# Kernel optimization log

Measured on AMD Instinct MI355X. Metric: run time of the kernel, lower is better.

Reference implementation:

```python
import jax, jax.numpy as jnp
import numpy as np

E = 128    # embedding_size
N = 8192   # total vertices (64 graphs x 128)
CN = 512   # total color slots
G = 64     # number of graphs
TMAX = 32


def _mlp3(x, W, b):
    # 3-layer MLP: Linear-ReLU-Linear-ReLU-Linear. W: [3,E,E], b: [3,E]
    h = jax.nn.relu(x @ W[0].T + b[0])
    h = jax.nn.relu(h @ W[1].T + b[1])
    return h @ W[2].T + b[2]


def _lstm_cell(x, h, c, Wih, Whh, bih, bhh):
    # PyTorch LSTM gate order: i, f, g, o
    gates = x @ Wih.T + h @ Whh.T + (bih + bhh)
    i, f, g, o = jnp.split(gates, 4, axis=-1)
    c2 = jax.nn.sigmoid(f) * c + jax.nn.sigmoid(i) * jnp.tanh(g)
    h2 = jax.nn.sigmoid(o) * jnp.tanh(c2)
    return h2, c2


def setup_inputs() -> dict:
    key = jax.random.key(0)
    ks = jax.random.split(key, 24)
    s = 1.0 / np.sqrt(E)
    f32 = jnp.float32
    inp = {
        "M_vv": jax.random.normal(ks[0], (N, N), f32) * s,
        "M_vc": jax.random.uniform(ks[1], (N, CN), f32) * (1.0 / np.sqrt(CN)),
        "C": jax.random.normal(ks[2], (CN, E), f32),
        "slice_idx": jnp.full((G,), N // G, dtype=jnp.int32),
        "v_emb_w": jax.random.normal(ks[3], (E, 1), f32) * s,
        "v_emb_b": jax.random.normal(ks[4], (E,), f32) * s,
        "mlpC_W": jax.random.normal(ks[5], (3, E, E), f32) * s,
        "mlpC_b": jax.random.normal(ks[6], (3, E), f32) * s,
        "mlpV_W": jax.random.normal(ks[7], (3, E, E), f32) * s,
        "mlpV_b": jax.random.normal(ks[8], (3, E), f32) * s,
        "Wih_v": jax.random.normal(ks[9], (4 * E, 2 * E), f32) * s,
        "Whh_v": jax.random.normal(ks[10], (4 * E, E), f32) * s,
        "bih_v": jax.random.normal(ks[11], (4 * E,), f32) * s,
        "bhh_v": jax.random.normal(ks[12], (4 * E,), f32) * s,
        "Wih_c": jax.random.normal(ks[13], (4 * E, E), f32) * s,
        "Whh_c": jax.random.normal(ks[14], (4 * E, E), f32) * s,
        "bih_c": jax.random.normal(ks[15], (4 * E,), f32) * s,
        "bhh_c": jax.random.normal(ks[16], (4 * E,), f32) * s,
        "vote_W1": jax.random.normal(ks[17], (E, E), f32) * s,
        "vote_b1": jax.random.normal(ks[18], (E,), f32) * s,
        "vote_W2": jax.random.normal(ks[19], (E, E), f32) * s,
        "vote_b2": jax.random.normal(ks[20], (E,), f32) * s,
        "vote_W3": jax.random.normal(ks[21], (1, E), f32) * s,
        "vote_b3": jax.random.normal(ks[22], (1,), f32) * s,
    }
    return inp


def reference(M_vv, M_vc, C, slice_idx, v_emb_w, v_emb_b, mlpC_W, mlpC_b,
              mlpV_W, mlpV_b, Wih_v, Whh_v, bih_v, bhh_v, Wih_c, Whh_c,
              bih_c, bhh_c, vote_W1, vote_b1, vote_W2, vote_b2, vote_W3, vote_b3):
    n = M_vv.shape[0]
    g = slice_idx.shape[0]
    # V = v_emb(ones(1)) broadcast to all vertices: [N, E]
    v0 = v_emb_w[:, 0] + v_emb_b
    V = jnp.broadcast_to(v0, (n, E))
    # Original torch loop never reassigns V, so both LSTM inputs are
    # loop-invariant; compute them once (identical math, no recompute).
    x_v = jnp.concatenate([M_vv @ V, M_vc @ _mlp3(C, mlpC_W, mlpC_b)], axis=1)  # [N, 2E]
    x_c = M_vc.T @ _mlp3(V, mlpV_W, mlpV_b)                                      # [CN, E]

    def step(carry, _):
        hv, cv, hc, cc = carry
        hv, cv = _lstm_cell(x_v, hv, cv, Wih_v, Whh_v, bih_v, bhh_v)
        hc, cc = _lstm_cell(x_c, hc, cc, Wih_c, Whh_c, bih_c, bhh_c)
        return (hv, cv, hc, cc), None

    init = (V, jnp.zeros_like(V), C, jnp.zeros_like(C))
    (hv, cv, hc, cc), _ = jax.lax.scan(step, init, None, length=TMAX)

    # vote MLP on final vertex hidden state -> [N, 1]
    h = jax.nn.relu(hv @ vote_W1.T + vote_b1)
    h = jax.nn.relu(h @ vote_W2.T + vote_b2)
    v_vote = (h @ vote_W3.T + vote_b3)[:, 0]  # [N]

    # per-graph mean then sigmoid (torch: split + mean + sigmoid + vstack)
    seg = jnp.repeat(jnp.arange(g), slice_idx, total_repeat_length=n)
    sums = jax.ops.segment_sum(v_vote, seg, num_segments=g)
    ret = jax.nn.sigmoid(sums / slice_idx.astype(sums.dtype))
    return (ret, V[None], C)
```

## Files before the change

### kernel.cpp

```cpp
#include <hip/hip_runtime.h>
#include <hip/hip_bf16.h>
#include <stdint.h>


typedef __bf16 bf16x8 __attribute__((ext_vector_type(8)));
typedef float f32x4 __attribute__((ext_vector_type(4)));

#define EDIM 128
#define NVERT 8192
#define CNUM 512
#define NG 64
#define TSTEPS 32

#define WS_RS 0u
#define WS_V0 32768u
#define WS_W1 33280u
#define WS_BV 35328u
#define WS_ACC 37376u
#define WS_V0BF 37632u
#define WS_MLPC3T 38912u

__device__ __forceinline__ float bf2f(unsigned short s) {
  return __uint_as_float(((unsigned)s) << 16);
}
__device__ __forceinline__ unsigned short f2bf(float f) {
  unsigned u = __float_as_uint(f);
  u += 0x7fffu + ((u >> 16) & 1u);
  return (unsigned short)(u >> 16);
}
__device__ __forceinline__ float sigm(float x) {
  return __builtin_amdgcn_rcpf(1.f + __expf(-x));
}
__device__ __forceinline__ float tanh_f(float x) {
  return 1.f - 2.f * __builtin_amdgcn_rcpf(1.f + __expf(2.f * x));
}
__device__ __forceinline__ f32x4 mfma16(bf16x8 a, bf16x8 b, f32x4 c) {
  return __builtin_amdgcn_mfma_f32_16x16x32_bf16(a, b, c, 0, 0, 0);
}
__device__ __forceinline__ bf16x8 ld8(const float* p) {
  float4 a = *(const float4*)p;
  float4 b = *(const float4*)(p + 4);
  bf16x8 r;
  r[0] = (__bf16)a.x; r[1] = (__bf16)a.y; r[2] = (__bf16)a.z; r[3] = (__bf16)a.w;
  r[4] = (__bf16)b.x; r[5] = (__bf16)b.y; r[6] = (__bf16)b.z; r[7] = (__bf16)b.w;
  return r;
}

__global__ __launch_bounds__(256) void k_rowsum(
    const float* __restrict__ M, float* __restrict__ rs) {
  const int row = blockIdx.x;
  const float4* p = (const float4*)(M + (size_t)row * NVERT);
  float s = 0.f;
#pragma unroll
  for (int it = 0; it < 8; it++) {
    float4 q = p[it * 256 + threadIdx.x];
    s += q.x + q.y + q.z + q.w;
  }
#pragma unroll
  for (int off = 32; off > 0; off >>= 1) s += __shfl_down(s, off, 64);
  __shared__ float red[4];
  if ((threadIdx.x & 63) == 0) red[threadIdx.x >> 6] = s;
  __syncthreads();
  if (threadIdx.x == 0) rs[row] = red[0] + red[1] + red[2] + red[3];
}

__global__ __launch_bounds__(512) void k_prep(
    const float* __restrict__ vw, const float* __restrict__ vb,
    const float* __restrict__ Wih,
    const float* __restrict__ bih, const float* __restrict__ bhh,
    float* __restrict__ ws) {
  __shared__ float v0s[EDIM];
  const int t = threadIdx.x;
  float* v0 = (float*)((char*)ws + WS_V0);
  float* w1 = (float*)((char*)ws + WS_W1);
  float* bv = (float*)((char*)ws + WS_BV);
  float* acc = (float*)((char*)ws + WS_ACC);
  unsigned short* v0bf = (unsigned short*)((char*)ws + WS_V0BF);
  if (t < EDIM) {
    float v = vw[t] + vb[t];
    v0s[t] = v;
    v0[t] = v;
    v0bf[t] = f2bf(v);
  }
  if (t < NG) acc[t] = 0.f;
  __syncthreads();
  {
    const float4* wr = (const float4*)(Wih + (size_t)t * 256);
    float s = 0.f;
#pragma unroll
    for (int kc = 0; kc < 32; kc++) {
      float4 q = wr[kc];
      const float* xi = v0s + kc * 4;
      s += q.x * xi[0] + q.y * xi[1] + q.z * xi[2] + q.w * xi[3];
    }
    w1[t] = s;
    bv[t] = bih[t] + bhh[t];
  }
}

__global__ __launch_bounds__(128) void k_mlpc(
    const float* __restrict__ C, const float* __restrict__ W,
    const float* __restrict__ B, float* __restrict__ ws) {
  unsigned short* out_t = (unsigned short*)((char*)ws + WS_MLPC3T);
  const int c = blockIdx.x, e = threadIdx.x;
  __shared__ float xb[2][EDIM];
  xb[0][e] = C[c * EDIM + e];
  __syncthreads();
#pragma unroll
  for (int l = 0; l < 3; l++) {
    const float4* wrow = (const float4*)(W + ((size_t)l * EDIM + e) * EDIM);
    const float* xin = xb[l & 1];
    float s = B[l * EDIM + e];
#pragma unroll
    for (int kc = 0; kc < EDIM / 4; kc++) {
      float4 q = wrow[kc];
      const float* xi = xin + kc * 4;
      s += q.x * xi[0] + q.y * xi[1] + q.z * xi[2] + q.w * xi[3];
    }
    if (l < 2) {
      s = fmaxf(s, 0.f);
      __syncthreads();
      xb[(l + 1) & 1][e] = s;
      __syncthreads();
    } else {
      out_t[(size_t)e * CNUM + c] = f2bf(s);
    }
  }
}

__global__ __launch_bounds__(256) void k_bcast(
    const float* __restrict__ ws, const float* __restrict__ Cin,
    float* __restrict__ out) {
  const float4* v0v = (const float4*)((const char*)ws + WS_V0);
  float4* Vout = (float4*)(out + NG);
  float4* Cout = (float4*)(out + NG + NVERT * EDIM);
  const float4* Cv = (const float4*)Cin;
  const int NVCH = (NVERT * EDIM) / 4;
  const int CCH = (CNUM * EDIM) / 4;
  int u = blockIdx.x * 256 + threadIdx.x;
  if (u < NVCH) Vout[u] = v0v[u & 31];
  else if (u < NVCH + CCH) Cout[u - NVCH] = Cv[u - NVCH];
}

__global__ __launch_bounds__(256, 1) void k_lstm(
    const float* __restrict__ Mvc, const float* __restrict__ Wih,
    const float* __restrict__ Whh,
    const float* __restrict__ W1, const float* __restrict__ b1,
    const float* __restrict__ W2, const float* __restrict__ b2,
    const float* __restrict__ W3, const float* __restrict__ b3,
    float* __restrict__ ws) {
  const int r0 = blockIdx.x * 32;
  const int t = threadIdx.x;
  const int w = t >> 6;
  const int lane = t & 63;
  const int quad = lane >> 4;
  const int l15 = lane & 15;
  const int nc0 = w * 32;

  __shared__ unsigned short Avc[32][CNUM + 8];
  __shared__ unsigned short Tt[32][EDIM + 8];
  __shared__ unsigned short hvs[32][EDIM + 8];
  __shared__ float votes[32];

  const float* rs = (const float*)((const char*)ws + WS_RS);
  const float* w1v = (const float*)((const char*)ws + WS_W1);
  const float* bvv = (const float*)((const char*)ws + WS_BV);
  float* accg = (float*)((char*)ws + WS_ACC);
  const unsigned short* v0bf = (const unsigned short*)((const char*)ws + WS_V0BF);
  const unsigned short* m3t = (const unsigned short*)((const char*)ws + WS_MLPC3T);

  {
    const int row = t >> 3, c0 = t & 7;
    const float4* g = (const float4*)(Mvc + (size_t)(r0 + row) * CNUM);
#pragma unroll
    for (int it = 0; it < 16; it++) {
      int c4 = it * 8 + c0;
      float4 q = g[c4];
      ushort4 h;
      h.x = f2bf(q.x); h.y = f2bf(q.y); h.z = f2bf(q.z); h.w = f2bf(q.w);
      *(ushort4*)&Avc[row][c4 * 4] = h;
    }
  }
  for (int i = t; i < 32 * EDIM; i += 256) hvs[i >> 7][i & 127] = v0bf[i & 127];
  __syncthreads();

  {
    f32x4 acc[2][2];
#pragma unroll
    for (int mt = 0; mt < 2; mt++)
#pragma unroll
      for (int ns = 0; ns < 2; ns++) {
        acc[mt][ns][0] = 0.f; acc[mt][ns][1] = 0.f;
        acc[mt][ns][2] = 0.f; acc[mt][ns][3] = 0.f;
      }
#pragma unroll
    for (int kc = 0; kc < 16; kc++) {
      bf16x8 a0 = *(const bf16x8*)&Avc[l15][kc * 32 + quad * 8];
      bf16x8 a1 = *(const bf16x8*)&Avc[16 + l15][kc * 32 + quad * 8];
      bf16x8 b0 = *(const bf16x8*)&m3t[(size_t)(nc0 + l15) * CNUM + kc * 32 + quad * 8];
      bf16x8 b1f = *(const bf16x8*)&m3t[(size_t)(nc0 + 16 + l15) * CNUM + kc * 32 + quad * 8];
      acc[0][0] = mfma16(a0, b0, acc[0][0]);
      acc[1][0] = mfma16(a1, b0, acc[1][0]);
      acc[0][1] = mfma16(a0, b1f, acc[0][1]);
      acc[1][1] = mfma16(a1, b1f, acc[1][1]);
    }
#pragma unroll
    for (int mt = 0; mt < 2; mt++)
#pragma unroll
      for (int ns = 0; ns < 2; ns++)
#pragma unroll
        for (int r = 0; r < 4; r++)
          Tt[mt * 16 + quad * 4 + r][nc0 + ns * 16 + l15] = f2bf(acc[mt][ns][r]);
  }
  __syncthreads();

  f32x4 xg[2][4][2];
  {
    float rsv[2][4];
#pragma unroll
    for (int mt = 0; mt < 2; mt++)
#pragma unroll
      for (int r = 0; r < 4; r++) rsv[mt][r] = rs[r0 + mt * 16 + quad * 4 + r];
#pragma unroll
    for (int gi = 0; gi < 4; gi++)
#pragma unroll
      for (int ns = 0; ns < 2; ns++) {
        const int col = gi * 128 + nc0 + ns * 16 + l15;
        const float w1c = w1v[col], bvc = bvv[col];
#pragma unroll
        for (int mt = 0; mt < 2; mt++)
#pragma unroll
          for (int r = 0; r < 4; r++) xg[mt][gi][ns][r] = fmaf(rsv[mt][r], w1c, bvc);
      }
#pragma unroll
    for (int kc = 0; kc < 4; kc++) {
      bf16x8 a0 = *(const bf16x8*)&Tt[l15][kc * 32 + quad * 8];
      bf16x8 a1 = *(const bf16x8*)&Tt[16 + l15][kc * 32 + quad * 8];
#pragma unroll
      for (int gi = 0; gi < 4; gi++)
#pragma unroll
        for (int ns = 0; ns < 2; ns++) {
          const int gcol = gi * 128 + nc0 + ns * 16 + l15;
          bf16x8 bfr = ld8(&Wih[(size_t)gcol * 256 + 128 + kc * 32 + quad * 8]);
          xg[0][gi][ns] = mfma16(a0, bfr, xg[0][gi][ns]);
          xg[1][gi][ns] = mfma16(a1, bfr, xg[1][gi][ns]);
        }
    }
  }

  bf16x8 Bh[4][2][4];
#pragma unroll
  for (int gi = 0; gi < 4; gi++)
#pragma unroll
    for (int ns = 0; ns < 2; ns++) {
      const int gcol = gi * 128 + nc0 + ns * 16 + l15;
#pragma unroll
      for (int kc = 0; kc < 4; kc++)
        Bh[gi][ns][kc] = ld8(&Whh[(size_t)gcol * EDIM + kc * 32 + quad * 8]);
    }

  f32x4 cv[2][2];
#pragma unroll
  for (int mt = 0; mt < 2; mt++)
#pragma unroll
    for (int ns = 0; ns < 2; ns++) {
      cv[mt][ns][0] = 0.f; cv[mt][ns][1] = 0.f;
      cv[mt][ns][2] = 0.f; cv[mt][ns][3] = 0.f;
    }

#pragma unroll 1
  for (int step = 0; step < TSTEPS; step++) {
    bf16x8 A[2][4];
#pragma unroll
    for (int mt = 0; mt < 2; mt++)
#pragma unroll
      for (int kc = 0; kc < 4; kc++)
        A[mt][kc] = *(const bf16x8*)&hvs[mt * 16 + l15][kc * 32 + quad * 8];
    __syncthreads();
#pragma unroll
    for (int mt = 0; mt < 2; mt++)
#pragma unroll
      for (int ns = 0; ns < 2; ns++) {
        f32x4 gI = xg[mt][0][ns], gF = xg[mt][1][ns];
        f32x4 gG = xg[mt][2][ns], gO = xg[mt][3][ns];
#pragma unroll
        for (int kc = 0; kc < 4; kc++) {
          gI = mfma16(A[mt][kc], Bh[0][ns][kc], gI);
          gF = mfma16(A[mt][kc], Bh[1][ns][kc], gF);
          gG = mfma16(A[mt][kc], Bh[2][ns][kc], gG);
          gO = mfma16(A[mt][kc], Bh[3][ns][kc], gO);
        }
#pragma unroll
        for (int r = 0; r < 4; r++) {
          float ig = sigm(gI[r]), fg = sigm(gF[r]);
          float gg = tanh_f(gG[r]), og = sigm(gO[r]);
          float c2 = fmaf(fg, cv[mt][ns][r], ig * gg);
          cv[mt][ns][r] = c2;
          hvs[mt * 16 + quad * 4 + r][nc0 + ns * 16 + l15] = f2bf(og * tanh_f(c2));
        }
      }
    __syncthreads();
  }

  for (int layer = 0; layer < 2; layer++) {
    const float* Wg = layer ? W2 : W1;
    const float* bg = layer ? b2 : b1;
    bf16x8 A[2][4];
#pragma unroll
    for (int mt = 0; mt < 2; mt++)
#pragma unroll
      for (int kc = 0; kc < 4; kc++)
        A[mt][kc] = *(const bf16x8*)&hvs[mt * 16 + l15][kc * 32 + quad * 8];
    f32x4 acc[2][2];
#pragma unroll
    for (int ns = 0; ns < 2; ns++) {
      float bb = bg[nc0 + ns * 16 + l15];
#pragma unroll
      for (int mt = 0; mt < 2; mt++) {
        acc[mt][ns][0] = bb; acc[mt][ns][1] = bb;
        acc[mt][ns][2] = bb; acc[mt][ns][3] = bb;
      }
    }
#pragma unroll
    for (int kc = 0; kc < 4; kc++)
#pragma unroll
      for (int ns = 0; ns < 2; ns++) {
        bf16x8 bfr = ld8(&Wg[(size_t)(nc0 + ns * 16 + l15) * EDIM + kc * 32 + quad * 8]);
        acc[0][ns] = mfma16(A[0][kc], bfr, acc[0][ns]);
        acc[1][ns] = mfma16(A[1][kc], bfr, acc[1][ns]);
      }
    __syncthreads();
#pragma unroll
    for (int mt = 0; mt < 2; mt++)
#pragma unroll
      for (int ns = 0; ns < 2; ns++)
#pragma unroll
        for (int r = 0; r < 4; r++)
          hvs[mt * 16 + quad * 4 + r][nc0 + ns * 16 + l15] = f2bf(fmaxf(acc[mt][ns][r], 0.f));
    __syncthreads();
  }

  {
    const int row = t >> 3, seg = t & 7;
    float part = 0.f;
#pragma unroll
    for (int j = 0; j < 16; j++) {
      const int k = seg * 16 + j;
      part += bf2f(hvs[row][k]) * W3[k];
    }
    part += __shfl_down(part, 4, 8);
    part += __shfl_down(part, 2, 8);
    part += __shfl_down(part, 1, 8);
    if ((t & 7) == 0) votes[row] = part + b3[0];
    __syncthreads();
    if (t < 64) {
      float v = (t < 32) ? votes[t] : 0.f;
#pragma unroll
      for (int off = 32; off > 0; off >>= 1) v += __shfl_down(v, off, 64);
      if (t == 0) atomicAdd(&accg[blockIdx.x >> 2], v);
    }
  }
}

__global__ __launch_bounds__(64) void k_final(const float* __restrict__ ws,
                                              const int* __restrict__ slice,
                                              float* __restrict__ out) {
  const float* accg = (const float*)((const char*)ws + WS_ACC);
  const int g = threadIdx.x;
  float m = accg[g] / (float)slice[g];
  out[g] = 1.f / (1.f + __expf(-m));
}

extern "C" void kernel_launch(void* const* d_in, const int* in_sizes, int n_in,
                              void* d_out, int out_size, void* d_ws, size_t ws_size,
                              hipStream_t stream) {
  const float* M_vv = (const float*)d_in[0];
  const float* M_vc = (const float*)d_in[1];
  const float* C = (const float*)d_in[2];
  const int* slice = (const int*)d_in[3];
  const float* vw = (const float*)d_in[4];
  const float* vb = (const float*)d_in[5];
  const float* mW = (const float*)d_in[6];
  const float* mB = (const float*)d_in[7];
  const float* Wih = (const float*)d_in[10];
  const float* Whh = (const float*)d_in[11];
  const float* bih = (const float*)d_in[12];
  const float* bhh = (const float*)d_in[13];
  const float* W1 = (const float*)d_in[18];
  const float* b1 = (const float*)d_in[19];
  const float* W2 = (const float*)d_in[20];
  const float* b2 = (const float*)d_in[21];
  const float* W3 = (const float*)d_in[22];
  const float* b3 = (const float*)d_in[23];
  float* ws = (float*)d_ws;
  float* out = (float*)d_out;

  k_rowsum<<<NVERT, 256, 0, stream>>>(M_vv, (float*)((char*)ws + WS_RS));
  k_prep<<<1, 512, 0, stream>>>(vw, vb, Wih, bih, bhh, ws);
  k_mlpc<<<CNUM, 128, 0, stream>>>(C, mW, mB, ws);
  k_bcast<<<1088, 256, 0, stream>>>(ws, C, out);
  k_lstm<<<256, 256, 0, stream>>>(M_vc, Wih, Whh, W1, b1, W2, b2, W3, b3, ws);
  k_final<<<1, 64, 0, stream>>>(ws, slice, out);
}
```

Baseline: 521.7 us.

## Fold output broadcast into rowsum/mlpc, double-buffer LSTM hidden, use 8 waves

Removes the separate broadcast kernel by writing the V output rows inside the rowsum kernel and the C copy inside the MLP kernel, with prep reordered to run first so V0 is ready. The LSTM kernel moves from 4 to 8 waves per block, each wave owning 16 columns instead of 32, which halves per-wave MFMA work and register footprint per step. The hidden state is double-buffered in shared memory so each timestep needs one barrier instead of two. This trades more shared memory and a larger block for shorter per-step latency on a recurrence bound by serial steps.

```diff
diff --git a/kernel.cpp b/kernel.cpp
--- a/kernel.cpp
+++ b/kernel.cpp
@@ -47,7 +47,8 @@
 }
 
 __global__ __launch_bounds__(256) void k_rowsum(
-    const float* __restrict__ M, float* __restrict__ rs) {
+    const float* __restrict__ M, const float* __restrict__ v0,
+    float* __restrict__ rs, float* __restrict__ Vout) {
   const int row = blockIdx.x;
   const float4* p = (const float4*)(M + (size_t)row * NVERT);
   float s = 0.f;
@@ -56,6 +57,9 @@
     float4 q = p[it * 256 + threadIdx.x];
     s += q.x + q.y + q.z + q.w;
   }
+  if (threadIdx.x < 32)
+    ((float4*)(Vout + (size_t)row * EDIM))[threadIdx.x] =
+        ((const float4*)v0)[threadIdx.x];
 #pragma unroll
   for (int off = 32; off > 0; off >>= 1) s += __shfl_down(s, off, 64);
   __shared__ float red[4];
@@ -100,11 +104,14 @@
 
 __global__ __launch_bounds__(128) void k_mlpc(
     const float* __restrict__ C, const float* __restrict__ W,
-    const float* __restrict__ B, float* __restrict__ ws) {
+    const float* __restrict__ B, float* __restrict__ ws,
+    float* __restrict__ Cout) {
   unsigned short* out_t = (unsigned short*)((char*)ws + WS_MLPC3T);
   const int c = blockIdx.x, e = threadIdx.x;
   __shared__ float xb[2][EDIM];
-  xb[0][e] = C[c * EDIM + e];
+  float cval = C[c * EDIM + e];
+  xb[0][e] = cval;
+  Cout[c * EDIM + e] = cval;
   __syncthreads();
 #pragma unroll
   for (int l = 0; l < 3; l++) {
@@ -128,21 +135,7 @@
   }
 }
 
-__global__ __launch_bounds__(256) void k_bcast(
-    const float* __restrict__ ws, const float* __restrict__ Cin,
-    float* __restrict__ out) {
-  const float4* v0v = (const float4*)((const char*)ws + WS_V0);
-  float4* Vout = (float4*)(out + NG);
-  float4* Cout = (float4*)(out + NG + NVERT * EDIM);
-  const float4* Cv = (const float4*)Cin;
-  const int NVCH = (NVERT * EDIM) / 4;
-  const int CCH = (CNUM * EDIM) / 4;
-  int u = blockIdx.x * 256 + threadIdx.x;
-  if (u < NVCH) Vout[u] = v0v[u & 31];
-  else if (u < NVCH + CCH) Cout[u - NVCH] = Cv[u - NVCH];
-}
-
-__global__ __launch_bounds__(256, 1) void k_lstm(
+__global__ __launch_bounds__(512, 1) void k_lstm(
     const float* __restrict__ Mvc, const float* __restrict__ Wih,
     const float* __restrict__ Whh,
     const float* __restrict__ W1, const float* __restrict__ b1,
@@ -155,11 +148,11 @@
   const int lane = t & 63;
   const int quad = lane >> 4;
   const int l15 = lane & 15;
-  const int nc0 = w * 32;
+  const int nc0 = w * 16;
 
   __shared__ unsigned short Avc[32][CNUM + 8];
   __shared__ unsigned short Tt[32][EDIM + 8];
-  __shared__ unsigned short hvs[32][EDIM + 8];
+  __shared__ unsigned short hv2[2][32][EDIM + 8];
   __shared__ float votes[32];
 
   const float* rs = (const float*)((const char*)ws + WS_RS);
@@ -170,51 +163,43 @@
   const unsigned short* m3t = (const unsigned short*)((const char*)ws + WS_MLPC3T);
 
   {
-    const int row = t >> 3, c0 = t & 7;
+    const int row = t >> 4, c0 = t & 15;
     const float4* g = (const float4*)(Mvc + (size_t)(r0 + row) * CNUM);
 #pragma unroll
-    for (int it = 0; it < 16; it++) {
-      int c4 = it * 8 + c0;
+    for (int it = 0; it < 8; it++) {
+      int c4 = it * 16 + c0;
       float4 q = g[c4];
       ushort4 h;
       h.x = f2bf(q.x); h.y = f2bf(q.y); h.z = f2bf(q.z); h.w = f2bf(q.w);
       *(ushort4*)&Avc[row][c4 * 4] = h;
     }
   }
-  for (int i = t; i < 32 * EDIM; i += 256) hvs[i >> 7][i & 127] = v0bf[i & 127];
-  __syncthreads();
-
-  {
-    f32x4 acc[2][2];
-#pragma unroll
-    for (int mt = 0; mt < 2; mt++)
-#pragma unroll
-      for (int ns = 0; ns < 2; ns++) {
-        acc[mt][ns][0] = 0.f; acc[mt][ns][1] = 0.f;
-        acc[mt][ns][2] = 0.f; acc[mt][ns][3] = 0.f;
-      }
+  for (int i = t; i < 32 * EDIM; i += 512) hv2[0][i >> 7][i & 127] = v0bf[i & 127];
+  __syncthreads();
+
+  {
+    f32x4 acc[2];
+#pragma unroll
+    for (int mt = 0; mt < 2; mt++) {
+      acc[mt][0] = 0.f; acc[mt][1] = 0.f; acc[mt][2] = 0.f; acc[mt][3] = 0.f;
+    }
 #pragma unroll
     for (int kc = 0; kc < 16; kc++) {
       bf16x8 a0 = *(const bf16x8*)&Avc[l15][kc * 32 + quad * 8];
       bf16x8 a1 = *(const bf16x8*)&Avc[16 + l15][kc * 32 + quad * 8];
       bf16x8 b0 = *(const bf16x8*)&m3t[(size_t)(nc0 + l15) * CNUM + kc * 32 + quad * 8];
-      bf16x8 b1f = *(const bf16x8*)&m3t[(size_t)(nc0 + 16 + l15) * CNUM + kc * 32 + quad * 8];
-      acc[0][0] = mfma16(a0, b0, acc[0][0]);
-      acc[1][0] = mfma16(a1, b0, acc[1][0]);
-      acc[0][1] = mfma16(a0, b1f, acc[0][1]);
-      acc[1][1] = mfma16(a1, b1f, acc[1][1]);
-    }
-#pragma unroll
-    for (int mt = 0; mt < 2; mt++)
-#pragma unroll
-      for (int ns = 0; ns < 2; ns++)
-#pragma unroll
-        for (int r = 0; r < 4; r++)
-          Tt[mt * 16 + quad * 4 + r][nc0 + ns * 16 + l15] = f2bf(acc[mt][ns][r]);
-  }
-  __syncthreads();
-
-  f32x4 xg[2][4][2];
+      acc[0] = mfma16(a0, b0, acc[0]);
+      acc[1] = mfma16(a1, b0, acc[1]);
+    }
+#pragma unroll
+    for (int mt = 0; mt < 2; mt++)
+#pragma unroll
+      for (int r = 0; r < 4; r++)
+        Tt[mt * 16 + quad * 4 + r][nc0 + l15] = f2bf(acc[mt][r]);
+  }
+  __syncthreads();
+
+  f32x4 xg[2][4];
   {
     float rsv[2][4];
 #pragma unroll
@@ -222,52 +207,44 @@
 #pragma unroll
       for (int r = 0; r < 4; r++) rsv[mt][r] = rs[r0 + mt * 16 + quad * 4 + r];
 #pragma unroll
-    for (int gi = 0; gi < 4; gi++)
-#pragma unroll
-      for (int ns = 0; ns < 2; ns++) {
-        const int col = gi * 128 + nc0 + ns * 16 + l15;
-        const float w1c = w1v[col], bvc = bvv[col];
-#pragma unroll
-        for (int mt = 0; mt < 2; mt++)
-#pragma unroll
-          for (int r = 0; r < 4; r++) xg[mt][gi][ns][r] = fmaf(rsv[mt][r], w1c, bvc);
-      }
+    for (int gi = 0; gi < 4; gi++) {
+      const int col = gi * 128 + nc0 + l15;
+      const float w1c = w1v[col], bvc = bvv[col];
+#pragma unroll
+      for (int mt = 0; mt < 2; mt++)
+#pragma unroll
+        for (int r = 0; r < 4; r++) xg[mt][gi][r] = fmaf(rsv[mt][r], w1c, bvc);
+    }
 #pragma unroll
     for (int kc = 0; kc < 4; kc++) {
       bf16x8 a0 = *(const bf16x8*)&Tt[l15][kc * 32 + quad * 8];
       bf16x8 a1 = *(const bf16x8*)&Tt[16 + l15][kc * 32 + quad * 8];
 #pragma unroll
-      for (int gi = 0; gi < 4; gi++)
-#pragma unroll
-        for (int ns = 0; ns < 2; ns++) {
-          const int gcol = gi * 128 + nc0 + ns * 16 + l15;
-          bf16x8 bfr = ld8(&Wih[(size_t)gcol * 256 + 128 + kc * 32 + quad * 8]);
-          xg[0][gi][ns] = mfma16(a0, bfr, xg[0][gi][ns]);
-          xg[1][gi][ns] = mfma16(a1, bfr, xg[1][gi][ns]);
-        }
-    }
-  }
-
-  bf16x8 Bh[4][2][4];
-#pragma unroll
-  for (int gi = 0; gi < 4; gi++)
-#pragma unroll
-    for (int ns = 0; ns < 2; ns++) {
-      const int gcol = gi * 128 + nc0 + ns * 16 + l15;
-#pragma unroll
-      for (int kc = 0; kc < 4; kc++)
-        Bh[gi][ns][kc] = ld8(&Whh[(size_t)gcol * EDIM + kc * 32 + quad * 8]);
-    }
-
-  f32x4 cv[2][2];
-#pragma unroll
-  for (int mt = 0; mt < 2; mt++)
-#pragma unroll
-    for (int ns = 0; ns < 2; ns++) {
-      cv[mt][ns][0] = 0.f; cv[mt][ns][1] = 0.f;
-      cv[mt][ns][2] = 0.f; cv[mt][ns][3] = 0.f;
-    }
-
+      for (int gi = 0; gi < 4; gi++) {
+        const int gcol = gi * 128 + nc0 + l15;
+        bf16x8 bfr = ld8(&Wih[(size_t)gcol * 256 + 128 + kc * 32 + quad * 8]);
+        xg[0][gi] = mfma16(a0, bfr, xg[0][gi]);
+        xg[1][gi] = mfma16(a1, bfr, xg[1][gi]);
+      }
+    }
+  }
+
+  bf16x8 Bh[4][4];
+#pragma unroll
+  for (int gi = 0; gi < 4; gi++) {
+    const int gcol = gi * 128 + nc0 + l15;
+#pragma unroll
+    for (int kc = 0; kc < 4; kc++)
+      Bh[gi][kc] = ld8(&Whh[(size_t)gcol * EDIM + kc * 32 + quad * 8]);
+  }
+
+  f32x4 cv[2];
+#pragma unroll
+  for (int mt = 0; mt < 2; mt++) {
+    cv[mt][0] = 0.f; cv[mt][1] = 0.f; cv[mt][2] = 0.f; cv[mt][3] = 0.f;
+  }
+
+  int p = 0;
 #pragma unroll 1
   for (int step = 0; step < TSTEPS; step++) {
     bf16x8 A[2][4];
@@ -275,30 +252,27 @@
     for (int mt = 0; mt < 2; mt++)
 #pragma unroll
       for (int kc = 0; kc < 4; kc++)
-        A[mt][kc] = *(const bf16x8*)&hvs[mt * 16 + l15][kc * 32 + quad * 8];
-    __syncthreads();
-#pragma unroll
-    for (int mt = 0; mt < 2; mt++)
-#pragma unroll
-      for (int ns = 0; ns < 2; ns++) {
-        f32x4 gI = xg[mt][0][ns], gF = xg[mt][1][ns];
-        f32x4 gG = xg[mt][2][ns], gO = xg[mt][3][ns];
-#pragma unroll
-        for (int kc = 0; kc < 4; kc++) {
-          gI = mfma16(A[mt][kc], Bh[0][ns][kc], gI);
-          gF = mfma16(A[mt][kc], Bh[1][ns][kc], gF);
-          gG = mfma16(A[mt][kc], Bh[2][ns][kc], gG);
-          gO = mfma16(A[mt][kc], Bh[3][ns][kc], gO);
-        }
-#pragma unroll
-        for (int r = 0; r < 4; r++) {
-          float ig = sigm(gI[r]), fg = sigm(gF[r]);
-          float gg = tanh_f(gG[r]), og = sigm(gO[r]);
-          float c2 = fmaf(fg, cv[mt][ns][r], ig * gg);
-          cv[mt][ns][r] = c2;
-          hvs[mt * 16 + quad * 4 + r][nc0 + ns * 16 + l15] = f2bf(og * tanh_f(c2));
-        }
+        A[mt][kc] = *(const bf16x8*)&hv2[p][mt * 16 + l15][kc * 32 + quad * 8];
+#pragma unroll
+    for (int mt = 0; mt < 2; mt++) {
+      f32x4 gI = xg[mt][0], gF = xg[mt][1], gG = xg[mt][2], gO = xg[mt][3];
+#pragma unroll
+      for (int kc = 0; kc < 4; kc++) {
+        gI = mfma16(A[mt][kc], Bh[0][kc], gI);
+        gF = mfma16(A[mt][kc], Bh[1][kc], gF);
+        gG = mfma16(A[mt][kc], Bh[2][kc], gG);
+        gO = mfma16(A[mt][kc], Bh[3][kc], gO);
       }
+#pragma unroll
+      for (int r = 0; r < 4; r++) {
+        float ig = sigm(gI[r]), fg = sigm(gF[r]);
+        float gg = tanh_f(gG[r]), og = sigm(gO[r]);
+        float c2 = fmaf(fg, cv[mt][r], ig * gg);
+        cv[mt][r] = c2;
+        hv2[p ^ 1][mt * 16 + quad * 4 + r][nc0 + l15] = f2bf(og * tanh_f(c2));
+      }
+    }
+    p ^= 1;
     __syncthreads();
   }
 
@@ -310,48 +284,43 @@
     for (int mt = 0; mt < 2; mt++)
 #pragma unroll
       for (int kc = 0; kc < 4; kc++)
-        A[mt][kc] = *(const bf16x8*)&hvs[mt * 16 + l15][kc * 32 + quad * 8];
-    f32x4 acc[2][2];
-#pragma unroll
-    for (int ns = 0; ns < 2; ns++) {
-      float bb = bg[nc0 + ns * 16 + l15];
+        A[mt][kc] = *(const bf16x8*)&hv2[0][mt * 16 + l15][kc * 32 + quad * 8];
+    f32x4 acc[2];
+    {
+      float bb = bg[nc0 + l15];
 #pragma unroll
       for (int mt = 0; mt < 2; mt++) {
-        acc[mt][ns][0] = bb; acc[mt][ns][1] = bb;
-        acc[mt][ns][2] = bb; acc[mt][ns][3] = bb;
+        acc[mt][0] = bb; acc[mt][1] = bb; acc[mt][2] = bb; acc[mt][3] = bb;
       }
     }
 #pragma unroll
-    for (int kc = 0; kc < 4; kc++)
-#pragma unroll
-      for (int ns = 0; ns < 2; ns++) {
-        bf16x8 bfr = ld8(&Wg[(size_t)(nc0 + ns * 16 + l15) * EDIM + kc * 32 + quad * 8]);
-        acc[0][ns] = mfma16(A[0][kc], bfr, acc[0][ns]);
-        acc[1][ns] = mfma16(A[1][kc], bfr, acc[1][ns]);
-      }
+    for (int kc = 0; kc < 4; kc++) {
+      bf16x8 bfr = ld8(&Wg[(size_t)(nc0 + l15) * EDIM + kc * 32 + quad * 8]);
+      acc[0] = mfma16(A[0][kc], bfr, acc[0]);
+      acc[1] = mfma16(A[1][kc], bfr, acc[1]);
+    }
     __syncthreads();
 #pragma unroll
     for (int mt = 0; mt < 2; mt++)
 #pragma unroll
-      for (int ns = 0; ns < 2; ns++)
-#pragma unroll
-        for (int r = 0; r < 4; r++)
-          hvs[mt * 16 + quad * 4 + r][nc0 + ns * 16 + l15] = f2bf(fmaxf(acc[mt][ns][r], 0.f));
+      for (int r = 0; r < 4; r++)
+        hv2[0][mt * 16 + quad * 4 + r][nc0 + l15] = f2bf(fmaxf(acc[mt][r], 0.f));
     __syncthreads();
   }
 
   {
-    const int row = t >> 3, seg = t & 7;
+    const int row = t >> 4, seg = t & 15;
     float part = 0.f;
 #pragma unroll
-    for (int j = 0; j < 16; j++) {
-      const int k = seg * 16 + j;
-      part += bf2f(hvs[row][k]) * W3[k];
-    }
-    part += __shfl_down(part, 4, 8);
-    part += __shfl_down(part, 2, 8);
-    part += __shfl_down(part, 1, 8);
-    if ((t & 7) == 0) votes[row] = part + b3[0];
+    for (int j = 0; j < 8; j++) {
+      const int k = seg * 8 + j;
+      part += bf2f(hv2[0][row][k]) * W3[k];
+    }
+    part += __shfl_down(part, 8, 16);
+    part += __shfl_down(part, 4, 16);
+    part += __shfl_down(part, 2, 16);
+    part += __shfl_down(part, 1, 16);
+    if (seg == 0) votes[row] = part + b3[0];
     __syncthreads();
     if (t < 64) {
       float v = (t < 32) ? votes[t] : 0.f;
@@ -395,10 +364,10 @@
   float* ws = (float*)d_ws;
   float* out = (float*)d_out;
 
-  k_rowsum<<<NVERT, 256, 0, stream>>>(M_vv, (float*)((char*)ws + WS_RS));
   k_prep<<<1, 512, 0, stream>>>(vw, vb, Wih, bih, bhh, ws);
-  k_mlpc<<<CNUM, 128, 0, stream>>>(C, mW, mB, ws);
-  k_bcast<<<1088, 256, 0, stream>>>(ws, C, out);
-  k_lstm<<<256, 256, 0, stream>>>(M_vc, Wih, Whh, W1, b1, W2, b2, W3, b3, ws);
+  k_rowsum<<<NVERT, 256, 0, stream>>>(M_vv, (const float*)((char*)ws + WS_V0),
+                                      (float*)((char*)ws + WS_RS), out + NG);
+  k_mlpc<<<CNUM, 128, 0, stream>>>(C, mW, mB, ws, out + NG + NVERT * EDIM);
+  k_lstm<<<256, 512, 0, stream>>>(M_vc, Wih, Whh, W1, b1, W2, b2, W3, b3, ws);
   k_final<<<1, 64, 0, stream>>>(ws, slice, out);
 }
```

Result: no change. 514.0 us (-1.5%).
